# Kernel optimization log

Hardware: AMD Instinct MI355X
Metric: run time of the kernel (lower is better)

The kernel has to match this reference:

```python
import jax, jax.numpy as jnp
import numpy as np

D_MODEL = 64
D_STATE = 16
D_CONV = 4
EXPAND = 2
D_INNER = EXPAND * D_MODEL        # 128
DT_RANK = max(1, D_MODEL // 16)   # 4 (mamba_ssm default ceil(d_model/16))
BATCH, HH, WW = 2, 128, 128


def setup_inputs() -> dict:
    key = jax.random.key(0)
    ks = jax.random.split(key, 10)
    def norm(k, shape, sc=0.05):
        return jax.random.normal(k, shape, jnp.float32) * sc
    # A initialized as in mamba_ssm: A = 1..d_state per channel, stored as log
    A_log = jnp.log(jnp.tile(jnp.arange(1, D_STATE + 1, dtype=jnp.float32), (4, D_INNER, 1)))
    return {
        "x": jax.random.normal(ks[0], (BATCH, D_MODEL, HH, WW), jnp.float32),
        "in_w": norm(ks[1], (4, 2 * D_INNER, D_MODEL)),
        "conv_w": norm(ks[2], (4, D_INNER, D_CONV), 0.2),
        "conv_b": jnp.zeros((4, D_INNER), jnp.float32),
        "xp_w": norm(ks[3], (4, DT_RANK + 2 * D_STATE, D_INNER)),
        "dtp_w": norm(ks[4], (4, D_INNER, DT_RANK), 0.2),
        "dtp_b": jnp.full((4, D_INNER), -4.0, jnp.float32) + norm(ks[5], (4, D_INNER), 0.5),
        "A_log": A_log,
        "Dp": jnp.ones((4, D_INNER), jnp.float32),
        "out_w": norm(ks[6], (4, D_MODEL, D_INNER)),
        "fuse_w": norm(ks[7], (D_MODEL, 4 * D_MODEL)),
        "fuse_b": jnp.zeros((D_MODEL,), jnp.float32),
        "ln_g": jnp.ones((D_MODEL,), jnp.float32),
        "ln_b": jnp.zeros((D_MODEL,), jnp.float32),
    }


def _mamba(xseq, in_w, conv_w, conv_b, xp_w, dtp_w, dtp_b, A_log, Dp, out_w):
    # xseq: (N, L, d_model) -> (N, L, d_model). Single-direction Mamba block.
    N, L, _ = xseq.shape
    xz = xseq @ in_w.T                       # (N, L, 2*d_inner)
    u, z = jnp.split(xz, 2, axis=-1)
    # causal depthwise conv1d, kernel width D_CONV
    up = jnp.pad(u, ((0, 0), (D_CONV - 1, 0), (0, 0)))
    uc = conv_b + sum(up[:, k:k + L, :] * conv_w[:, k][None, None, :] for k in range(D_CONV))
    uc = jax.nn.silu(uc)
    dbl = uc @ xp_w.T                        # (N, L, dt_rank + 2*d_state)
    dt = jax.nn.softplus(dbl[..., :DT_RANK] @ dtp_w.T + dtp_b)   # (N, L, d_inner)
    Bm = dbl[..., DT_RANK:DT_RANK + D_STATE]                     # (N, L, d_state)
    Cm = dbl[..., DT_RANK + D_STATE:]                            # (N, L, d_state)
    A = -jnp.exp(A_log)                                          # (d_inner, d_state)

    def step(h, inp):
        dt_t, B_t, C_t, u_t = inp            # (N,d_inner),(N,d_state),(N,d_state),(N,d_inner)
        h = h * jnp.exp(dt_t[..., None] * A) + (dt_t * u_t)[..., None] * B_t[:, None, :]
        y = jnp.einsum('nds,ns->nd', h, C_t)
        return h, y

    h0 = jnp.zeros((N, D_INNER, D_STATE), xseq.dtype)
    _, ys = jax.lax.scan(step, h0, (dt.swapaxes(0, 1), Bm.swapaxes(0, 1),
                                    Cm.swapaxes(0, 1), uc.swapaxes(0, 1)))
    y = ys.swapaxes(0, 1) + uc * Dp
    y = y * jax.nn.silu(z)
    return y @ out_w.T


def reference(x, in_w, conv_w, conv_b, xp_w, dtp_w, dtp_b, A_log, Dp, out_w,
              fuse_w, fuse_b, ln_g, ln_b):
    B, C, H, W = x.shape
    xhwc = x.transpose(0, 2, 3, 1)           # (B,H,W,C)
    xwhc = x.transpose(0, 3, 2, 1)           # (B,W,H,C)
    d0 = xhwc.reshape(B * H, W, C)                         # horizontal fwd
    d1 = xhwc[:, :, ::-1, :].reshape(B * H, W, C)          # horizontal bwd
    d2 = xwhc.reshape(B * W, H, C)                         # vertical fwd
    d3 = xwhc[:, :, ::-1, :].reshape(B * W, H, C)          # vertical bwd
    xd = jnp.stack([d0, d1, d2, d3])         # (4, B*S, S, C) since H == W
    ys = jax.vmap(_mamba)(xd, in_w, conv_w, conv_b, xp_w, dtp_w, dtp_b, A_log, Dp, out_w)
    y0 = ys[0].reshape(B, H, W, C)
    y1 = ys[1].reshape(B, H, W, C)[:, :, ::-1, :]
    y2 = ys[2].reshape(B, W, H, C).transpose(0, 2, 1, 3)
    y3 = ys[3].reshape(B, W, H, C)[:, :, ::-1, :].transpose(0, 2, 1, 3)
    cat = jnp.concatenate([y0, y1, y2, y3], axis=-1)       # (B,H,W,4C)
    f = cat @ fuse_w.T + fuse_b                            # 1x1 conv
    mu = f.mean(-1, keepdims=True)
    var = f.var(-1, keepdims=True)
    f = (f - mu) * jax.lax.rsqrt(var + 1e-5) * ln_g + ln_b # LayerNorm over C
    f = jax.nn.silu(f)
    return f.transpose(0, 3, 1, 2)                          # (B,C,H,W)
```

## Files before the change

### kernel.cpp

```cpp
#include <hip/hip_runtime.h>
#include <hip/hip_bf16.h>
#include <math.h>


typedef __attribute__((ext_vector_type(8))) short short8;
typedef __attribute__((ext_vector_type(4))) float f32x4;
typedef __attribute__((ext_vector_type(2))) float f32x2;

__device__ __forceinline__ f32x2 pk_mul(f32x2 a, f32x2 b) {
  f32x2 d;
  asm("v_pk_mul_f32 %0, %1, %2" : "=v"(d) : "v"(a), "v"(b));
  return d;
}
__device__ __forceinline__ f32x2 pk_fma(f32x2 a, f32x2 b, f32x2 c) {
  f32x2 d;
  asm("v_pk_fma_f32 %0, %1, %2, %3" : "=v"(d) : "v"(a), "v"(b), "v"(c));
  return d;
}

__device__ __forceinline__ unsigned int pk2bf(float a, float b) {
  __hip_bfloat162 h = __float22bfloat162_rn(make_float2(a, b));
  unsigned int u;
  __builtin_memcpy(&u, &h, 4);
  return u;
}
__device__ __forceinline__ unsigned short f2bf(float f) {
  __hip_bfloat16 h = __float2bfloat16(f);
  unsigned short s;
  __builtin_memcpy(&s, &h, 2);
  return s;
}
__device__ __forceinline__ float bf2f(unsigned short h) {
  return __uint_as_float(((unsigned int)h) << 16);
}
__device__ __forceinline__ float fastrcp(float x) { return __builtin_amdgcn_rcpf(x); }
__device__ __forceinline__ float siluf(float x) { return x * fastrcp(1.f + __expf(-x)); }

__global__ void k0_prep(const float* __restrict__ out_w, const float* __restrict__ fuse_w,
                        const float* __restrict__ in_w, const float* __restrict__ xp_w,
                        const float* __restrict__ x,
                        unsigned short* __restrict__ MT16, unsigned short* __restrict__ W16,
                        unsigned short* __restrict__ XW16, unsigned short* __restrict__ XH,
                        unsigned short* __restrict__ XW) {
  __shared__ unsigned short sT[64*132];
  int blk = blockIdx.x;
  int tid = threadIdx.x;
  if (blk < 128) {
    int idx = blk * 256 + tid;
    int d   = idx & 127;
    int o   = (idx >> 7) & 63;
    int dir = idx >> 13;
    float acc = 0.f;
    #pragma unroll 8
    for (int j = 0; j < 64; ++j)
      acc += out_w[(dir*64 + j)*128 + d] * fuse_w[o*256 + dir*64 + j];
    MT16[o*512 + dir*128 + d] = f2bf(acc);
  } else if (blk < 160) {
    int t = (blk - 128) * 256 + tid;
    int base = t * 8;
    float4 v0 = *(const float4*)(in_w + base);
    float4 v1 = *(const float4*)(in_w + base + 4);
    uint4 pk;
    pk.x = pk2bf(v0.x, v0.y);
    pk.y = pk2bf(v0.z, v0.w);
    pk.z = pk2bf(v1.x, v1.y);
    pk.w = pk2bf(v1.z, v1.w);
    *(uint4*)(W16 + base) = pk;
  } else if (blk < 164) {
    int t = (blk - 160) * 256 + tid;
    for (int pid = t; pid < 4*48*128; pid += 1024) {
      int dir = pid / 6144;
      int rem = pid - dir*6144;
      int row = rem >> 7, c = rem & 127;
      XW16[pid] = (row < 36) ? f2bf(xp_w[dir*4608 + row*128 + c]) : (unsigned short)0;
    }
  } else {
    int idx = blk - 164;
    int b = idx >> 7, h = idx & 127;
    for (int f = tid*4; f < 8192; f += 1024) {
      int c = f >> 7, w = f & 127;
      float4 v = *(const float4*)(x + (((size_t)(b*64 + c)*128 + h)*128 + w));
      sT[c*132 + w + 0] = f2bf(v.x);
      sT[c*132 + w + 1] = f2bf(v.y);
      sT[c*132 + w + 2] = f2bf(v.z);
      sT[c*132 + w + 3] = f2bf(v.w);
    }
    __syncthreads();
    for (int f = tid*8; f < 8192; f += 2048) {
      int w = f >> 6, c0 = f & 63;
      unsigned int pk[4];
      #pragma unroll
      for (int p = 0; p < 4; ++p) {
        unsigned int lo = sT[(c0 + p*2 + 0)*132 + w];
        unsigned int hi = sT[(c0 + p*2 + 1)*132 + w];
        pk[p] = lo | (hi << 16);
      }
      uint4 v; v.x = pk[0]; v.y = pk[1]; v.z = pk[2]; v.w = pk[3];
      *(uint4*)(XH + (((size_t)(b*128 + h)*128 + w)*64 + c0)) = v;
      *(uint4*)(XW + (((size_t)(b*128 + w)*128 + h)*64 + c0)) = v;
    }
  }
}

__global__ __launch_bounds__(256, 3) void k1_front(
    const unsigned short* __restrict__ XH, const unsigned short* __restrict__ XW,
    const unsigned short* __restrict__ W16, const unsigned short* __restrict__ XW16,
    const float* __restrict__ conv_w, const float* __restrict__ conv_b,
    const float* __restrict__ dtp_w, const float* __restrict__ dtp_b,
    const float* __restrict__ A_log, const float* __restrict__ Dp,
    unsigned short* __restrict__ YF)
{
  __shared__ __align__(16) char smem[53248];
  float* sBCf         = (float*)smem;
  unsigned short* sUC = (unsigned short*)(smem + 18432);

  const int tid = threadIdx.x;
  const int dir = blockIdx.x >> 8;
  const int n   = blockIdx.x & 255;
  const int b   = n >> 7;
  const int r   = n & 127;
  const int n_all = dir*256 + n;

  const unsigned short* xsrc = (dir < 2 ? XH : XW) + ((size_t)(b*128 + r)*128)*64;

  const int wave = tid >> 6;
  const int lane = tid & 63;
  const int m16 = lane & 15;
  const int quad = lane >> 4;
  const int tb0 = wave * 32;
  const int st0 = tb0 + m16;
  const int st1 = tb0 + 16 + m16;
  const int sp0 = (dir & 1) ? (127 - st0) : st0;
  const int sp1 = (dir & 1) ? (127 - st1) : st1;

  unsigned int zpk[2][8][2];

  {
    short8 bfr[2][2];
    #pragma unroll
    for (int ks = 0; ks < 2; ++ks) {
      bfr[0][ks] = *(const short8*)(xsrc + sp0*64 + ks*32 + quad*8);
      bfr[1][ks] = *(const short8*)(xsrc + sp1*64 + ks*32 + quad*8);
    }
    const unsigned short* Wd = W16 + (size_t)dir * 16384;

    for (int rt = 0; rt < 8; ++rt) {
      short8 af[2];
      #pragma unroll
      for (int ks = 0; ks < 2; ++ks)
        af[ks] = *(const short8*)(Wd + (rt*16 + m16)*64 + ks*32 + quad*8);
      #pragma unroll
      for (int tt = 0; tt < 2; ++tt) {
        f32x4 acc = {0.f, 0.f, 0.f, 0.f};
        acc = __builtin_amdgcn_mfma_f32_16x16x32_bf16(af[0], bfr[tt][0], acc, 0, 0, 0);
        acc = __builtin_amdgcn_mfma_f32_16x16x32_bf16(af[1], bfr[tt][1], acc, 0, 0, 0);
        const int tok = tt ? st1 : st0;
        const int r0 = rt*16 + quad*4;
        uint2 u2;
        u2.x = pk2bf(acc[0], acc[1]);
        u2.y = pk2bf(acc[2], acc[3]);
        *(uint2*)(sUC + tok*136 + r0) = u2;
      }
    }
    #pragma unroll
    for (int k = 0; k < 8; ++k) {
      short8 af[2];
      #pragma unroll
      for (int ks = 0; ks < 2; ++ks)
        af[ks] = *(const short8*)(Wd + ((8+k)*16 + m16)*64 + ks*32 + quad*8);
      #pragma unroll
      for (int tt = 0; tt < 2; ++tt) {
        f32x4 acc = {0.f, 0.f, 0.f, 0.f};
        acc = __builtin_amdgcn_mfma_f32_16x16x32_bf16(af[0], bfr[tt][0], acc, 0, 0, 0);
        acc = __builtin_amdgcn_mfma_f32_16x16x32_bf16(af[1], bfr[tt][1], acc, 0, 0, 0);
        zpk[tt][k][0] = pk2bf(siluf(acc[0]), siluf(acc[1]));
        zpk[tt][k][1] = pk2bf(siluf(acc[2]), siluf(acc[3]));
      }
    }
  }
  __syncthreads();

  {
    const int d = tid & 127;
    const int half = tid >> 7;
    const int ca = half * 32;
    const int cb2 = (half + 2) * 32;
    const float* cw = conv_w + (size_t)(dir*128 + d)*4;
    const float c0w = cw[0], c1w = cw[1], c2w = cw[2], c3w = cw[3];
    const float cbv = conv_b[dir*128 + d];
    const f32x2 cw0v = {c0w, c0w}, cw1v = {c1w, c1w}, cw2v = {c2w, c2w}, cw3v = {c3w, c3w};
    const f32x2 cbv2 = {cbv, cbv};
    f32x2 A0 = { half ? bf2f(sUC[(ca-3)*136 + d]) : 0.f, bf2f(sUC[(cb2-3)*136 + d]) };
    f32x2 A1 = { half ? bf2f(sUC[(ca-2)*136 + d]) : 0.f, bf2f(sUC[(cb2-2)*136 + d]) };
    f32x2 A2 = { half ? bf2f(sUC[(ca-1)*136 + d]) : 0.f, bf2f(sUC[(cb2-1)*136 + d]) };
    __syncthreads();
    unsigned short* pa = sUC + ca*136 + d;
    unsigned short* pb = sUC + cb2*136 + d;
    for (int i = 0; i < 32; ++i) {
      f32x2 cur = { bf2f(*pa), bf2f(*pb) };
      f32x2 v = pk_fma(cw3v, cur,
                pk_fma(cw2v, A2,
                pk_fma(cw1v, A1,
                pk_fma(cw0v, A0, cbv2))));
      *pa = f2bf(siluf(v.x));
      *pb = f2bf(siluf(v.y));
      A0 = A1; A1 = A2; A2 = cur;
      pa += 136; pb += 136;
    }
  }
  __syncthreads();

  {
    short8 bfr[2][4];
    #pragma unroll
    for (int tt = 0; tt < 2; ++tt)
      #pragma unroll
      for (int ks = 0; ks < 4; ++ks)
        bfr[tt][ks] = *(const short8*)(sUC + (tt ? st1 : st0)*136 + ks*32 + quad*8);

    const unsigned short* XWd = XW16 + (size_t)dir * (48*128);

    for (int rt = 0; rt < 3; ++rt) {
      short8 af[4];
      #pragma unroll
      for (int ks = 0; ks < 4; ++ks)
        af[ks] = *(const short8*)(XWd + (rt*16 + m16)*128 + ks*32 + quad*8);
      #pragma unroll
      for (int tt = 0; tt < 2; ++tt) {
        f32x4 acc = {0.f, 0.f, 0.f, 0.f};
        #pragma unroll
        for (int ks = 0; ks < 4; ++ks)
          acc = __builtin_amdgcn_mfma_f32_16x16x32_bf16(af[ks], bfr[tt][ks], acc, 0, 0, 0);
        const int tok = tt ? st1 : st0;
        const int r0 = rt*16 + quad*4;
        if (r0 == 0) {
          float4 v; v.x = acc[0]; v.y = acc[1]; v.z = acc[2]; v.w = acc[3];
          *(float4*)(smem + 18432 + tok*272 + 256) = v;
        } else if (r0 < 36) {
          float4 v; v.x = acc[0]; v.y = acc[1]; v.z = acc[2]; v.w = acc[3];
          *(float4*)(sBCf + tok*36 + (r0 - 4)) = v;
        }
      }
    }
  }
  __syncthreads();

  {
    const int d = tid >> 1;
    const int p = tid & 1;
    const float* dwp = dtp_w + (size_t)(dir*128 + d) * 4;
    const float dw0 = dwp[0], dw1 = dwp[1], dw2 = dwp[2], dw3 = dwp[3];
    const float db = dtp_b[dir*128 + d];
    const float dpv = Dp[dir*128 + d];

    float Av[8];
    bool fast = true;
    #pragma unroll
    for (int j = 0; j < 8; ++j) {
      float a = -__expf(A_log[((size_t)(dir*128 + d))*16 + p*8 + j]);
      Av[j] = a;
      if (fabsf((-a) - (float)(p*8 + j + 1)) > 1e-3f) fast = false;
    }

    if (fast) {
      f32x2 h0 = {0.f, 0.f}, h1 = {0.f, 0.f}, h2v = {0.f, 0.f}, h3 = {0.f, 0.f};
      const char* qp = smem + 18432 + 256;
      const float* bp = sBCf + p*8;
      const float* cp = sBCf + 16 + p*8;
      const unsigned short* up = sUC + d;
      unsigned short* yo = sUC + d;
      for (int l = 0; l < 128; ++l) {
        float4 Q = *(const float4*)qp;
        f32x2 B01 = *(const f32x2*)(bp + 0), B23 = *(const f32x2*)(bp + 2);
        f32x2 B45 = *(const f32x2*)(bp + 4), B67 = *(const f32x2*)(bp + 6);
        f32x2 C01 = *(const f32x2*)(cp + 0), C23 = *(const f32x2*)(cp + 2);
        f32x2 C45 = *(const f32x2*)(cp + 4), C67 = *(const f32x2*)(cp + 6);
        float u = bf2f(*up);
        float dr = Q.x*dw0 + Q.y*dw1 + Q.z*dw2 + Q.w*dw3 + db;
        float te = __expf(dr);
        float dt = (dr > 20.f) ? dr : __logf(1.f + te);
        float dtu = dt * u;
        float E = fastrcp(1.f + te);
        float E2 = E*E, E4 = E2*E2, E8 = E4*E4;
        float eb = p ? E8 : 1.f;
        f32x2 P0 = {E*eb, E2*eb};
        f32x2 E2v = {E2, E2};
        f32x2 P1 = pk_mul(P0, E2v);
        f32x2 P2 = pk_mul(P1, E2v);
        f32x2 P3 = pk_mul(P2, E2v);
        f32x2 du = {dtu, dtu};
        h0  = pk_fma(h0,  P0, pk_mul(du, B01));
        h1  = pk_fma(h1,  P1, pk_mul(du, B23));
        h2v = pk_fma(h2v, P2, pk_mul(du, B45));
        h3  = pk_fma(h3,  P3, pk_mul(du, B67));
        f32x2 ya = pk_mul(h0, C01);
        f32x2 yb = pk_mul(h1, C23);
        ya = pk_fma(h2v, C45, ya);
        yb = pk_fma(h3,  C67, yb);
        float ypar = (ya.x + ya.y) + (yb.x + yb.y);
        float ot = __uint_as_float((unsigned int)__builtin_amdgcn_mov_dpp(
                     (int)__float_as_uint(ypar), 0xB1, 0xF, 0xF, true));
        float ysum = ypar + ot;
        *yo = f2bf(ysum + u*dpv);
        qp += 272; bp += 36; cp += 36; up += 136; yo += 136;
      }
    } else {
      float h[8];
      #pragma unroll
      for (int j = 0; j < 8; ++j) h[j] = 0.f;
      for (int l = 0; l < 128; ++l) {
        float4 Q = *(const float4*)(smem + 18432 + l*272 + 256);
        float4 b0 = *(const float4*)(sBCf + l*36 + p*8);
        float4 b1 = *(const float4*)(sBCf + l*36 + p*8 + 4);
        float4 c0 = *(const float4*)(sBCf + l*36 + 16 + p*8);
        float4 c1 = *(const float4*)(sBCf + l*36 + 16 + p*8 + 4);
        float Bv[8] = {b0.x,b0.y,b0.z,b0.w, b1.x,b1.y,b1.z,b1.w};
        float Cv[8] = {c0.x,c0.y,c0.z,c0.w, c1.x,c1.y,c1.z,c1.w};
        float u = bf2f(sUC[l*136 + d]);
        float dr = Q.x*dw0 + Q.y*dw1 + Q.z*dw2 + Q.w*dw3 + db;
        float te = __expf(dr);
        float dt = (dr > 20.f) ? dr : __logf(1.f + te);
        float dtu = dt * u;
        float yp = 0.f;
        #pragma unroll
        for (int j = 0; j < 8; ++j) {
          float ej = __expf(dt*Av[j]);
          h[j] = h[j]*ej + dtu*Bv[j];
          yp += h[j]*Cv[j];
        }
        float ot = __uint_as_float((unsigned int)__builtin_amdgcn_mov_dpp(
                     (int)__float_as_uint(yp), 0xB1, 0xF, 0xF, true));
        float ysum = yp + ot;
        if (p == 0) sUC[l*136 + d] = f2bf(ysum + u*dpv);
      }
    }
  }
  __syncthreads();

  #pragma unroll
  for (int tt = 0; tt < 2; ++tt) {
    const int st = tt ? st1 : st0;
    size_t rowbase;
    if (dir < 2)       rowbase = ((size_t)n_all*128 + st)*128;
    else if (dir == 2) rowbase = ((size_t)(512 + b*128 + st)*128 + r)*128;
    else               rowbase = ((size_t)(768 + b*128 + (127-st))*128 + r)*128;
    #pragma unroll
    for (int k = 0; k < 8; ++k) {
      const int dz = 16*k + quad*4;
      uint2 yv = *(const uint2*)(sUC + st*136 + dz);
      float y0 = __uint_as_float(yv.x << 16);
      float y1 = __uint_as_float(yv.x & 0xffff0000u);
      float y2 = __uint_as_float(yv.y << 16);
      float y3 = __uint_as_float(yv.y & 0xffff0000u);
      unsigned int z01 = zpk[tt][k][0], z23 = zpk[tt][k][1];
      float z0 = __uint_as_float(z01 << 16);
      float z1 = __uint_as_float(z01 & 0xffff0000u);
      float z2 = __uint_as_float(z23 << 16);
      float z3 = __uint_as_float(z23 & 0xffff0000u);
      uint2 ov;
      ov.x = pk2bf(y0*z0, y1*z1);
      ov.y = pk2bf(y2*z2, y3*z3);
      *(uint2*)(YF + rowbase + dz) = ov;
    }
  }
}

__global__ __launch_bounds__(512, 2) void k3_fuse(
    const unsigned short* __restrict__ YF, const unsigned short* __restrict__ MT16,
    const float* __restrict__ fuse_b, const float* __restrict__ ln_g,
    const float* __restrict__ ln_b, float* __restrict__ out)
{
  __shared__ __align__(16) unsigned short sYB[64*520];
  __shared__ float sLN[2][64][2];

  const int tid = threadIdx.x;
  const int blk = blockIdx.x;
  const int b = blk >> 8;
  const int rr2 = blk & 255;
  const int h = rr2 >> 1;
  const int w0 = (rr2 & 1) * 64;

  for (int f = tid*8; f < 32768; f += 4096) {
    int dirg = f >> 13;
    int rem = f & 8191;
    int tok = rem >> 7;
    int dd = rem & 127;
    int X = (dirg == 1) ? (127 - w0 - tok) : (w0 + tok);
    size_t base = ((size_t)(dirg*256 + b*128 + h)*128 + X)*128 + dd;
    *(uint4*)(sYB + tok*520 + dirg*128 + dd) = *(const uint4*)(YF + base);
  }
  __syncthreads();

  const int wave = tid >> 6;
  const int lane = tid & 63;
  const int m16 = lane & 15;
  const int quad = lane >> 4;
  const int tg   = wave & 3;
  const int mh   = wave >> 2;
  const int tok  = tg*16 + m16;

  short8 bfr[16];
  #pragma unroll
  for (int jt = 0; jt < 16; ++jt)
    bfr[jt] = *(const short8*)(sYB + tok*520 + jt*32 + quad*8);

  float facc[2][4];
  #pragma unroll
  for (int mi = 0; mi < 2; ++mi) {
    const int mt = mh*2 + mi;
    f32x4 acc = {0.f, 0.f, 0.f, 0.f};
    #pragma unroll
    for (int jt = 0; jt < 16; ++jt) {
      short8 af = *(const short8*)(MT16 + (size_t)(mt*16 + m16)*512 + jt*32 + quad*8);
      acc = __builtin_amdgcn_mfma_f32_16x16x32_bf16(af, bfr[jt], acc, 0, 0, 0);
    }
// ... 13 lines not shown
    }
  s1 += __shfl_xor(s1, 16, 64); s1 += __shfl_xor(s1, 32, 64);
  s2 += __shfl_xor(s2, 16, 64); s2 += __shfl_xor(s2, 32, 64);
  if (lane < 16) {
    sLN[mh][tok][0] = s1;
    sLN[mh][tok][1] = s2;
  }
  __syncthreads();
  float t1 = s1 + sLN[1 - mh][tok][0];
  float t2 = s2 + sLN[1 - mh][tok][1];
  float mu = t1 * (1.f/64.f);
  float var = t2 * (1.f/64.f) - mu*mu;
  float rs = rsqrtf(var + 1e-5f);

  #pragma unroll
  for (int mi = 0; mi < 2; ++mi)
    #pragma unroll
    for (int rr = 0; rr < 4; ++rr) {
      int o = (mh*2 + mi)*16 + quad*4 + rr;
      float v = (fv[mi*4 + rr] - mu) * rs * ln_g[o] + ln_b[o];
      out[((size_t)(b*64 + o)*128 + h)*128 + (w0 + tok)] = siluf(v);
    }
}

extern "C" void kernel_launch(void* const* d_in, const int* in_sizes, int n_in,
                              void* d_out, int out_size, void* d_ws, size_t ws_size,
                              hipStream_t stream) {
  const float* x      = (const float*)d_in[0];
  const float* in_w   = (const float*)d_in[1];
  const float* conv_w = (const float*)d_in[2];
  const float* conv_b = (const float*)d_in[3];
  const float* xp_w   = (const float*)d_in[4];
  const float* dtp_w  = (const float*)d_in[5];
  const float* dtp_b  = (const float*)d_in[6];
  const float* A_log  = (const float*)d_in[7];
  const float* Dp     = (const float*)d_in[8];
  const float* out_w  = (const float*)d_in[9];
  const float* fuse_w = (const float*)d_in[10];
  const float* fuse_b = (const float*)d_in[11];
  const float* ln_g   = (const float*)d_in[12];
  const float* ln_b   = (const float*)d_in[13];
  float* out = (float*)d_out;

  char* ws = (char*)d_ws;
  unsigned short* YF   = (unsigned short*)(ws);
  unsigned short* MT16 = (unsigned short*)(ws + 33554432);
  unsigned short* W16  = (unsigned short*)(ws + 33619968);
  unsigned short* XW16 = (unsigned short*)(ws + 33751040);
  unsigned short* XH   = (unsigned short*)(ws + 33800192);
  unsigned short* XWt  = (unsigned short*)(ws + 37994496);

  k0_prep<<<dim3(420), dim3(256), 0, stream>>>(out_w, fuse_w, in_w, xp_w, x,
                                               MT16, W16, XW16, XH, XWt);
  k1_front<<<dim3(1024), dim3(256), 0, stream>>>(XH, XWt, W16, XW16, conv_w, conv_b,
                                                 dtp_w, dtp_b, A_log, Dp, YF);
  k3_fuse<<<dim3(512), dim3(512), 0, stream>>>(YF, MT16, fuse_b, ln_g, ln_b, out);
}
```

Before: 203.5 us.

## Process two sequences per k1_front block, hoisting per-direction params and x_proj weights

k1_front now launches 512 blocks, and each block loops over two sequences of the same direction. The per-direction parameters (conv weights, dt_proj, A, D) and the x_proj weight fragments are loaded into registers once per block instead of once per sequence. Launch bounds drop from 3 to 2 blocks per SM to make room for the extra live registers. The cost is less occupancy and parallelism: 512 blocks on 256 CUs at 2 per CU fill only a single wave, so latency hiding may suffer.

```diff
diff --git a/kernel.cpp b/kernel.cpp
--- a/kernel.cpp
+++ b/kernel.cpp
@@ -102,7 +102,7 @@
   }
 }
 
-__global__ __launch_bounds__(256, 3) void k1_front(
+__global__ __launch_bounds__(256, 2) void k1_front(
     const unsigned short* __restrict__ XH, const unsigned short* __restrict__ XW,
     const unsigned short* __restrict__ W16, const unsigned short* __restrict__ XW16,
     const float* __restrict__ conv_w, const float* __restrict__ conv_b,
@@ -115,13 +115,8 @@
   unsigned short* sUC = (unsigned short*)(smem + 18432);
 
   const int tid = threadIdx.x;
-  const int dir = blockIdx.x >> 8;
-  const int n   = blockIdx.x & 255;
-  const int b   = n >> 7;
-  const int r   = n & 127;
-  const int n_all = dir*256 + n;
-
-  const unsigned short* xsrc = (dir < 2 ? XH : XW) + ((size_t)(b*128 + r)*128)*64;
+  const int dir = blockIdx.x >> 7;
+  const int n2  = blockIdx.x & 127;
 
   const int wave = tid >> 6;
   const int lane = tid & 63;
@@ -130,237 +125,251 @@
   const int tb0 = wave * 32;
   const int st0 = tb0 + m16;
   const int st1 = tb0 + 16 + m16;
-  const int sp0 = (dir & 1) ? (127 - st0) : st0;
-  const int sp1 = (dir & 1) ? (127 - st1) : st1;
-
-  unsigned int zpk[2][8][2];
-
-  {
-    short8 bfr[2][2];
+
+  const int cd = tid & 127;
+  const float* cwp = conv_w + (size_t)(dir*128 + cd)*4;
+  const float c0w = cwp[0], c1w = cwp[1], c2w = cwp[2], c3w = cwp[3];
+  const float cbv = conv_b[dir*128 + cd];
+  const int sd = tid >> 1;
+  const int sp_ = tid & 1;
+  const float* dwp = dtp_w + (size_t)(dir*128 + sd) * 4;
+  const float dw0 = dwp[0], dw1 = dwp[1], dw2 = dwp[2], dw3 = dwp[3];
+  const float db = dtp_b[dir*128 + sd];
+  const float dpv = Dp[dir*128 + sd];
+  float Av[8];
+  bool fast = true;
+  #pragma unroll
+  for (int j = 0; j < 8; ++j) {
+    float a = -__expf(A_log[((size_t)(dir*128 + sd))*16 + sp_*8 + j]);
+    Av[j] = a;
+    if (fabsf((-a) - (float)(sp_*8 + j + 1)) > 1e-3f) fast = false;
+  }
+  const unsigned short* XWd = XW16 + (size_t)dir * (48*128);
+  short8 af4[3][4];
+  #pragma unroll
+  for (int rt = 0; rt < 3; ++rt)
     #pragma unroll
-    for (int ks = 0; ks < 2; ++ks) {
-      bfr[0][ks] = *(const short8*)(xsrc + sp0*64 + ks*32 + quad*8);
-      bfr[1][ks] = *(const short8*)(xsrc + sp1*64 + ks*32 + quad*8);
-    }
-    const unsigned short* Wd = W16 + (size_t)dir * 16384;
-
-    for (int rt = 0; rt < 8; ++rt) {
-      short8 af[2];
-      #pragma unroll
-      for (int ks = 0; ks < 2; ++ks)
-        af[ks] = *(const short8*)(Wd + (rt*16 + m16)*64 + ks*32 + quad*8);
-      #pragma unroll
-      for (int tt = 0; tt < 2; ++tt) {
-        f32x4 acc = {0.f, 0.f, 0.f, 0.f};
-        acc = __builtin_amdgcn_mfma_f32_16x16x32_bf16(af[0], bfr[tt][0], acc, 0, 0, 0);
-        acc = __builtin_amdgcn_mfma_f32_16x16x32_bf16(af[1], bfr[tt][1], acc, 0, 0, 0);
-        const int tok = tt ? st1 : st0;
-        const int r0 = rt*16 + quad*4;
-        uint2 u2;
-        u2.x = pk2bf(acc[0], acc[1]);
-        u2.y = pk2bf(acc[2], acc[3]);
-        *(uint2*)(sUC + tok*136 + r0) = u2;
-      }
-    }
+    for (int ks = 0; ks < 4; ++ks)
+      af4[rt][ks] = *(const short8*)(XWd + (rt*16 + m16)*128 + ks*32 + quad*8);
+
+  const unsigned short* Wd = W16 + (size_t)dir * 16384;
+
+  for (int half = 0; half < 2; ++half) {
+    const int n = n2 + half*128;
+    const int b = n >> 7;
+    const int r = n & 127;
+    const int n_all = dir*256 + n;
+    const unsigned short* xsrc = (dir < 2 ? XH : XW) + ((size_t)(b*128 + r)*128)*64;
+    const int sp0 = (dir & 1) ? (127 - st0) : st0;
+    const int sp1 = (dir & 1) ? (127 - st1) : st1;
+
+    if (half) __syncthreads();
+
+    unsigned int zpk[2][8][2];
+
+    {
+      short8 bfr[2][2];
+      #pragma unroll
+      for (int ks = 0; ks < 2; ++ks) {
+        bfr[0][ks] = *(const short8*)(xsrc + sp0*64 + ks*32 + quad*8);
+        bfr[1][ks] = *(const short8*)(xsrc + sp1*64 + ks*32 + quad*8);
+      }
+      for (int rt = 0; rt < 8; ++rt) {
+        short8 af[2];
+        #pragma unroll
+        for (int ks = 0; ks < 2; ++ks)
+          af[ks] = *(const short8*)(Wd + (rt*16 + m16)*64 + ks*32 + quad*8);
+        #pragma unroll
+        for (int tt = 0; tt < 2; ++tt) {
+          f32x4 acc = {0.f, 0.f, 0.f, 0.f};
+          acc = __builtin_amdgcn_mfma_f32_16x16x32_bf16(af[0], bfr[tt][0], acc, 0, 0, 0);
+          acc = __builtin_amdgcn_mfma_f32_16x16x32_bf16(af[1], bfr[tt][1], acc, 0, 0, 0);
+          const int tok = tt ? st1 : st0;
+          const int r0 = rt*16 + quad*4;
+          uint2 u2;
+          u2.x = pk2bf(acc[0], acc[1]);
+          u2.y = pk2bf(acc[2], acc[3]);
+          *(uint2*)(sUC + tok*136 + r0) = u2;
+        }
+      }
+      #pragma unroll
+      for (int k = 0; k < 8; ++k) {
+        short8 af[2];
+        #pragma unroll
+        for (int ks = 0; ks < 2; ++ks)
+          af[ks] = *(const short8*)(Wd + ((8+k)*16 + m16)*64 + ks*32 + quad*8);
+        #pragma unroll
+        for (int tt = 0; tt < 2; ++tt) {
+          f32x4 acc = {0.f, 0.f, 0.f, 0.f};
+          acc = __builtin_amdgcn_mfma_f32_16x16x32_bf16(af[0], bfr[tt][0], acc, 0, 0, 0);
+          acc = __builtin_amdgcn_mfma_f32_16x16x32_bf16(af[1], bfr[tt][1], acc, 0, 0, 0);
+          zpk[tt][k][0] = pk2bf(siluf(acc[0]), siluf(acc[1]));
+          zpk[tt][k][1] = pk2bf(siluf(acc[2]), siluf(acc[3]));
+        }
+      }
+    }
+    __syncthreads();
+
+    {
+      const int d = cd;
+      const int hlf = tid >> 7;
+      const int ca = hlf * 32;
+      const int cb2 = (hlf + 2) * 32;
+      const f32x2 cw0v = {c0w, c0w}, cw1v = {c1w, c1w}, cw2v = {c2w, c2w}, cw3v = {c3w, c3w};
+      const f32x2 cbv2 = {cbv, cbv};
+      f32x2 A0 = { hlf ? bf2f(sUC[(ca-3)*136 + d]) : 0.f, bf2f(sUC[(cb2-3)*136 + d]) };
+      f32x2 A1 = { hlf ? bf2f(sUC[(ca-2)*136 + d]) : 0.f, bf2f(sUC[(cb2-2)*136 + d]) };
+      f32x2 A2 = { hlf ? bf2f(sUC[(ca-1)*136 + d]) : 0.f, bf2f(sUC[(cb2-1)*136 + d]) };
+      __syncthreads();
+      unsigned short* pa = sUC + ca*136 + d;
+      unsigned short* pb = sUC + cb2*136 + d;
+      for (int i = 0; i < 32; ++i) {
+        f32x2 cur = { bf2f(*pa), bf2f(*pb) };
+        f32x2 v = pk_fma(cw3v, cur,
+                  pk_fma(cw2v, A2,
+                  pk_fma(cw1v, A1,
+                  pk_fma(cw0v, A0, cbv2))));
+        *pa = f2bf(siluf(v.x));
+        *pb = f2bf(siluf(v.y));
+        A0 = A1; A1 = A2; A2 = cur;
+        pa += 136; pb += 136;
+      }
+    }
+    __syncthreads();
+
+    {
+      short8 bfr[2][4];
+      #pragma unroll
+      for (int tt = 0; tt < 2; ++tt)
+        #pragma unroll
+        for (int ks = 0; ks < 4; ++ks)
+          bfr[tt][ks] = *(const short8*)(sUC + (tt ? st1 : st0)*136 + ks*32 + quad*8);
+
+      #pragma unroll
+      for (int rt = 0; rt < 3; ++rt) {
+        #pragma unroll
+        for (int tt = 0; tt < 2; ++tt) {
+          f32x4 acc = {0.f, 0.f, 0.f, 0.f};
+          #pragma unroll
+          for (int ks = 0; ks < 4; ++ks)
+            acc = __builtin_amdgcn_mfma_f32_16x16x32_bf16(af4[rt][ks], bfr[tt][ks], acc, 0, 0, 0);
+          const int tok = tt ? st1 : st0;
+          const int r0 = rt*16 + quad*4;
+          if (r0 == 0) {
+            float4 v; v.x = acc[0]; v.y = acc[1]; v.z = acc[2]; v.w = acc[3];
+            *(float4*)(smem + 18432 + tok*272 + 256) = v;
+          } else if (r0 < 36) {
+            float4 v; v.x = acc[0]; v.y = acc[1]; v.z = acc[2]; v.w = acc[3];
+            *(float4*)(sBCf + tok*36 + (r0 - 4)) = v;
+          }
+        }
+      }
+    }
+    __syncthreads();
+
+    {
+      const int d = sd;
+      const int p = sp_;
+      if (fast) {
+        f32x2 h0 = {0.f, 0.f}, h1 = {0.f, 0.f}, h2v = {0.f, 0.f}, h3 = {0.f, 0.f};
+        const char* qp = smem + 18432 + 256;
+        const float* bp = sBCf + p*8;
+        const float* cp = sBCf + 16 + p*8;
+        const unsigned short* up = sUC + d;
+        unsigned short* yo = sUC + d;
+        for (int l = 0; l < 128; ++l) {
+          float4 Q = *(const float4*)qp;
+          f32x2 B01 = *(const f32x2*)(bp + 0), B23 = *(const f32x2*)(bp + 2);
+          f32x2 B45 = *(const f32x2*)(bp + 4), B67 = *(const f32x2*)(bp + 6);
+          f32x2 C01 = *(const f32x2*)(cp + 0), C23 = *(const f32x2*)(cp + 2);
+          f32x2 C45 = *(const f32x2*)(cp + 4), C67 = *(const f32x2*)(cp + 6);
+          float u = bf2f(*up);
+          float dr = Q.x*dw0 + Q.y*dw1 + Q.z*dw2 + Q.w*dw3 + db;
+          float te = __expf(dr);
+          float dt = (dr > 20.f) ? dr : __logf(1.f + te);
+          float dtu = dt * u;
+          float E = fastrcp(1.f + te);
+          float E2 = E*E, E4 = E2*E2, E8 = E4*E4;
+          float eb = p ? E8 : 1.f;
+          f32x2 P0 = {E*eb, E2*eb};
+          f32x2 E2v = {E2, E2};
+          f32x2 P1 = pk_mul(P0, E2v);
+          f32x2 P2 = pk_mul(P1, E2v);
+          f32x2 P3 = pk_mul(P2, E2v);
+          f32x2 du = {dtu, dtu};
+          h0  = pk_fma(h0,  P0, pk_mul(du, B01));
+          h1  = pk_fma(h1,  P1, pk_mul(du, B23));
+          h2v = pk_fma(h2v, P2, pk_mul(du, B45));
+          h3  = pk_fma(h3,  P3, pk_mul(du, B67));
+          f32x2 ya = pk_mul(h0, C01);
+          f32x2 yb = pk_mul(h1, C23);
+          ya = pk_fma(h2v, C45, ya);
+          yb = pk_fma(h3,  C67, yb);
+          float ypar = (ya.x + ya.y) + (yb.x + yb.y);
+          float ot = __uint_as_float((unsigned int)__builtin_amdgcn_mov_dpp(
+                       (int)__float_as_uint(ypar), 0xB1, 0xF, 0xF, true));
+          float ysum = ypar + ot;
+          *yo = f2bf(ysum + u*dpv);
+          qp += 272; bp += 36; cp += 36; up += 136; yo += 136;
+        }
+      } else {
+        float h[8];
+        #pragma unroll
+        for (int j = 0; j < 8; ++j) h[j] = 0.f;
+        for (int l = 0; l < 128; ++l) {
+          float4 Q = *(const float4*)(smem + 18432 + l*272 + 256);
+          float4 b0 = *(const float4*)(sBCf + l*36 + p*8);
+          float4 b1 = *(const float4*)(sBCf + l*36 + p*8 + 4);
+          float4 c0 = *(const float4*)(sBCf + l*36 + 16 + p*8);
+          float4 c1 = *(const float4*)(sBCf + l*36 + 16 + p*8 + 4);
+          float Bv[8] = {b0.x,b0.y,b0.z,b0.w, b1.x,b1.y,b1.z,b1.w};
+          float Cv[8] = {c0.x,c0.y,c0.z,c0.w, c1.x,c1.y,c1.z,c1.w};
+          float u = bf2f(sUC[l*136 + d]);
+          float dr = Q.x*dw0 + Q.y*dw1 + Q.z*dw2 + Q.w*dw3 + db;
+          float te = __expf(dr);
+          float dt = (dr > 20.f) ? dr : __logf(1.f + te);
+          float dtu = dt * u;
+          float yp = 0.f;
+          #pragma unroll
+          for (int j = 0; j < 8; ++j) {
+            float ej = __expf(dt*Av[j]);
+            h[j] = h[j]*ej + dtu*Bv[j];
+            yp += h[j]*Cv[j];
+          }
+          float ot = __uint_as_float((unsigned int)__builtin_amdgcn_mov_dpp(
+                       (int)__float_as_uint(yp), 0xB1, 0xF, 0xF, true));
+          float ysum = yp + ot;
+          if (p == 0) sUC[l*136 + d] = f2bf(ysum + u*dpv);
+        }
+      }
+    }
+    __syncthreads();
+
     #pragma unroll
-    for (int k = 0; k < 8; ++k) {
-      short8 af[2];
-      #pragma unroll
-      for (int ks = 0; ks < 2; ++ks)
-        af[ks] = *(const short8*)(Wd + ((8+k)*16 + m16)*64 + ks*32 + quad*8);
-      #pragma unroll
-      for (int tt = 0; tt < 2; ++tt) {
-        f32x4 acc = {0.f, 0.f, 0.f, 0.f};
-        acc = __builtin_amdgcn_mfma_f32_16x16x32_bf16(af[0], bfr[tt][0], acc, 0, 0, 0);
-        acc = __builtin_amdgcn_mfma_f32_16x16x32_bf16(af[1], bfr[tt][1], acc, 0, 0, 0);
-        zpk[tt][k][0] = pk2bf(siluf(acc[0]), siluf(acc[1]));
-        zpk[tt][k][1] = pk2bf(siluf(acc[2]), siluf(acc[3]));
-      }
-    }
-  }
-  __syncthreads();
-
-  {
-    const int d = tid & 127;
-    const int half = tid >> 7;
-    const int ca = half * 32;
-    const int cb2 = (half + 2) * 32;
-    const float* cw = conv_w + (size_t)(dir*128 + d)*4;
-    const float c0w = cw[0], c1w = cw[1], c2w = cw[2], c3w = cw[3];
-    const float cbv = conv_b[dir*128 + d];
-    const f32x2 cw0v = {c0w, c0w}, cw1v = {c1w, c1w}, cw2v = {c2w, c2w}, cw3v = {c3w, c3w};
-    const f32x2 cbv2 = {cbv, cbv};
-    f32x2 A0 = { half ? bf2f(sUC[(ca-3)*136 + d]) : 0.f, bf2f(sUC[(cb2-3)*136 + d]) };
-    f32x2 A1 = { half ? bf2f(sUC[(ca-2)*136 + d]) : 0.f, bf2f(sUC[(cb2-2)*136 + d]) };
-    f32x2 A2 = { half ? bf2f(sUC[(ca-1)*136 + d]) : 0.f, bf2f(sUC[(cb2-1)*136 + d]) };
-    __syncthreads();
-    unsigned short* pa = sUC + ca*136 + d;
-    unsigned short* pb = sUC + cb2*136 + d;
-    for (int i = 0; i < 32; ++i) {
-      f32x2 cur = { bf2f(*pa), bf2f(*pb) };
-      f32x2 v = pk_fma(cw3v, cur,
-                pk_fma(cw2v, A2,
-                pk_fma(cw1v, A1,
-                pk_fma(cw0v, A0, cbv2))));
-      *pa = f2bf(siluf(v.x));
-      *pb = f2bf(siluf(v.y));
-      A0 = A1; A1 = A2; A2 = cur;
-      pa += 136; pb += 136;
-    }
-  }
-  __syncthreads();
-
-  {
-    short8 bfr[2][4];
-    #pragma unroll
-    for (int tt = 0; tt < 2; ++tt)
-      #pragma unroll
-      for (int ks = 0; ks < 4; ++ks)
-        bfr[tt][ks] = *(const short8*)(sUC + (tt ? st1 : st0)*136 + ks*32 + quad*8);
-
-    const unsigned short* XWd = XW16 + (size_t)dir * (48*128);
-
-    for (int rt = 0; rt < 3; ++rt) {
-      short8 af[4];
-      #pragma unroll
-      for (int ks = 0; ks < 4; ++ks)
-        af[ks] = *(const short8*)(XWd + (rt*16 + m16)*128 + ks*32 + quad*8);
-      #pragma unroll
-      for (int tt = 0; tt < 2; ++tt) {
-        f32x4 acc = {0.f, 0.f, 0.f, 0.f};
-        #pragma unroll
-        for (int ks = 0; ks < 4; ++ks)
-          acc = __builtin_amdgcn_mfma_f32_16x16x32_bf16(af[ks], bfr[tt][ks], acc, 0, 0, 0);
-        const int tok = tt ? st1 : st0;
-        const int r0 = rt*16 + quad*4;
-        if (r0 == 0) {
-          float4 v; v.x = acc[0]; v.y = acc[1]; v.z = acc[2]; v.w = acc[3];
-          *(float4*)(smem + 18432 + tok*272 + 256) = v;
-        } else if (r0 < 36) {
-          float4 v; v.x = acc[0]; v.y = acc[1]; v.z = acc[2]; v.w = acc[3];
-          *(float4*)(sBCf + tok*36 + (r0 - 4)) = v;
-        }
-      }
-    }
-  }
-  __syncthreads();
-
-  {
-    const int d = tid >> 1;
-    const int p = tid & 1;
-    const float* dwp = dtp_w + (size_t)(dir*128 + d) * 4;
-    const float dw0 = dwp[0], dw1 = dwp[1], dw2 = dwp[2], dw3 = dwp[3];
-    const float db = dtp_b[dir*128 + d];
-    const float dpv = Dp[dir*128 + d];
-
-    float Av[8];
-    bool fast = true;
-    #pragma unroll
-    for (int j = 0; j < 8; ++j) {
-      float a = -__expf(A_log[((size_t)(dir*128 + d))*16 + p*8 + j]);
-      Av[j] = a;
-      if (fabsf((-a) - (float)(p*8 + j + 1)) > 1e-3f) fast = false;
-    }
-
-    if (fast) {
-      f32x2 h0 = {0.f, 0.f}, h1 = {0.f, 0.f}, h2v = {0.f, 0.f}, h3 = {0.f, 0.f};
-      const char* qp = smem + 18432 + 256;
-      const float* bp = sBCf + p*8;
-      const float* cp = sBCf + 16 + p*8;
-      const unsigned short* up = sUC + d;
-      unsigned short* yo = sUC + d;
-      for (int l = 0; l < 128; ++l) {
-        float4 Q = *(const float4*)qp;
-        f32x2 B01 = *(const f32x2*)(bp + 0), B23 = *(const f32x2*)(bp + 2);
-        f32x2 B45 = *(const f32x2*)(bp + 4), B67 = *(const f32x2*)(bp + 6);
-        f32x2 C01 = *(const f32x2*)(cp + 0), C23 = *(const f32x2*)(cp + 2);
-        f32x2 C45 = *(const f32x2*)(cp + 4), C67 = *(const f32x2*)(cp + 6);
-        float u = bf2f(*up);
-        float dr = Q.x*dw0 + Q.y*dw1 + Q.z*dw2 + Q.w*dw3 + db;
-        float te = __expf(dr);
-        float dt = (dr > 20.f) ? dr : __logf(1.f + te);
-        float dtu = dt * u;
-        float E = fastrcp(1.f + te);
-        float E2 = E*E, E4 = E2*E2, E8 = E4*E4;
-        float eb = p ? E8 : 1.f;
-        f32x2 P0 = {E*eb, E2*eb};
-        f32x2 E2v = {E2, E2};
-        f32x2 P1 = pk_mul(P0, E2v);
-        f32x2 P2 = pk_mul(P1, E2v);
-        f32x2 P3 = pk_mul(P2, E2v);
-        f32x2 du = {dtu, dtu};
-        h0  = pk_fma(h0,  P0, pk_mul(du, B01));
-        h1  = pk_fma(h1,  P1, pk_mul(du, B23));
-        h2v = pk_fma(h2v, P2, pk_mul(du, B45));
-        h3  = pk_fma(h3,  P3, pk_mul(du, B67));
-        f32x2 ya = pk_mul(h0, C01);
-        f32x2 yb = pk_mul(h1, C23);
-        ya = pk_fma(h2v, C45, ya);
-        yb = pk_fma(h3,  C67, yb);
-        float ypar = (ya.x + ya.y) + (yb.x + yb.y);
-        float ot = __uint_as_float((unsigned int)__builtin_amdgcn_mov_dpp(
-                     (int)__float_as_uint(ypar), 0xB1, 0xF, 0xF, true));
-        float ysum = ypar + ot;
-        *yo = f2bf(ysum + u*dpv);
-        qp += 272; bp += 36; cp += 36; up += 136; yo += 136;
-      }
-    } else {
-      float h[8];
-      #pragma unroll
-      for (int j = 0; j < 8; ++j) h[j] = 0.f;
-      for (int l = 0; l < 128; ++l) {
-        float4 Q = *(const float4*)(smem + 18432 + l*272 + 256);
-        float4 b0 = *(const float4*)(sBCf + l*36 + p*8);
-        float4 b1 = *(const float4*)(sBCf + l*36 + p*8 + 4);
-        float4 c0 = *(const float4*)(sBCf + l*36 + 16 + p*8);
-        float4 c1 = *(const float4*)(sBCf + l*36 + 16 + p*8 + 4);
-        float Bv[8] = {b0.x,b0.y,b0.z,b0.w, b1.x,b1.y,b1.z,b1.w};
-        float Cv[8] = {c0.x,c0.y,c0.z,c0.w, c1.x,c1.y,c1.z,c1.w};
-        float u = bf2f(sUC[l*136 + d]);
-        float dr = Q.x*dw0 + Q.y*dw1 + Q.z*dw2 + Q.w*dw3 + db;
-        float te = __expf(dr);
-        float dt = (dr > 20.f) ? dr : __logf(1.f + te);
-        float dtu = dt * u;
-        float yp = 0.f;
-        #pragma unroll
-        for (int j = 0; j < 8; ++j) {
-          float ej = __expf(dt*Av[j]);
-          h[j] = h[j]*ej + dtu*Bv[j];
-          yp += h[j]*Cv[j];
-        }
-        float ot = __uint_as_float((unsigned int)__builtin_amdgcn_mov_dpp(
-                     (int)__float_as_uint(yp), 0xB1, 0xF, 0xF, true));
-        float ysum = yp + ot;
-        if (p == 0) sUC[l*136 + d] = f2bf(ysum + u*dpv);
-      }
-    }
-  }
-  __syncthreads();
-
-  #pragma unroll
-  for (int tt = 0; tt < 2; ++tt) {
-    const int st = tt ? st1 : st0;
-    size_t rowbase;
-    if (dir < 2)       rowbase = ((size_t)n_all*128 + st)*128;
-    else if (dir == 2) rowbase = ((size_t)(512 + b*128 + st)*128 + r)*128;
-    else               rowbase = ((size_t)(768 + b*128 + (127-st))*128 + r)*128;
-    #pragma unroll
-    for (int k = 0; k < 8; ++k) {
-      const int dz = 16*k + quad*4;
-      uint2 yv = *(const uint2*)(sUC + st*136 + dz);
-      float y0 = __uint_as_float(yv.x << 16);
-      float y1 = __uint_as_float(yv.x & 0xffff0000u);
-      float y2 = __uint_as_float(yv.y << 16);
-      float y3 = __uint_as_float(yv.y & 0xffff0000u);
-      unsigned int z01 = zpk[tt][k][0], z23 = zpk[tt][k][1];
-      float z0 = __uint_as_float(z01 << 16);
-      float z1 = __uint_as_float(z01 & 0xffff0000u);
-      float z2 = __uint_as_float(z23 << 16);
-      float z3 = __uint_as_float(z23 & 0xffff0000u);
-      uint2 ov;
-      ov.x = pk2bf(y0*z0, y1*z1);
-      ov.y = pk2bf(y2*z2, y3*z3);
-      *(uint2*)(YF + rowbase + dz) = ov;
+    for (int tt = 0; tt < 2; ++tt) {
+      const int st = tt ? st1 : st0;
+      size_t rowbase;
+      if (dir < 2)       rowbase = ((size_t)n_all*128 + st)*128;
+      else if (dir == 2) rowbase = ((size_t)(512 + b*128 + st)*128 + r)*128;
+      else               rowbase = ((size_t)(768 + b*128 + (127-st))*128 + r)*128;
+      #pragma unroll
+      for (int k = 0; k < 8; ++k) {
+        const int dz = 16*k + quad*4;
+        uint2 yv = *(const uint2*)(sUC + st*136 + dz);
+        float y0 = __uint_as_float(yv.x << 16);
+        float y1 = __uint_as_float(yv.x & 0xffff0000u);
+        float y2 = __uint_as_float(yv.y << 16);
+        float y3 = __uint_as_float(yv.y & 0xffff0000u);
+        unsigned int z01 = zpk[tt][k][0], z23 = zpk[tt][k][1];
+        float z0 = __uint_as_float(z01 << 16);
+        float z1 = __uint_as_float(z01 & 0xffff0000u);
+        float z2 = __uint_as_float(z23 << 16);
+        float z3 = __uint_as_float(z23 & 0xffff0000u);
+        uint2 ov;
+        ov.x = pk2bf(y0*z0, y1*z1);
+        ov.y = pk2bf(y2*z2, y3*z3);
+        *(uint2*)(YF + rowbase + dz) = ov;
+      }
     }
   }
 }
@@ -480,7 +489,7 @@
 
   k0_prep<<<dim3(420), dim3(256), 0, stream>>>(out_w, fuse_w, in_w, xp_w, x,
                                                MT16, W16, XW16, XH, XWt);
-  k1_front<<<dim3(1024), dim3(256), 0, stream>>>(XH, XWt, W16, XW16, conv_w, conv_b,
-                                                 dtp_w, dtp_b, A_log, Dp, YF);
+  k1_front<<<dim3(512), dim3(256), 0, stream>>>(XH, XWt, W16, XW16, conv_w, conv_b,
+                                                dtp_w, dtp_b, A_log, Dp, YF);
   k3_fuse<<<dim3(512), dim3(512), 0, stream>>>(YF, MT16, fuse_b, ln_g, ln_b, out);
 }
```

Result: slower. 246.8 us (+21.3%).

## Split selective scan into two sequence chunks with state carry-over correction

Applied to the files above, without the earlier changes.

Doubles k1_front block size to 512 threads so each wave handles 16 tokens instead of 32. The selective scan is split into two 64-token chunks run in parallel. The second chunk starts from zero state, and a correction pass then adds the first chunk's propagated final state using cumulative decay products. This relies on A being 1..16 so that exp(dt*A) equals powers of a single factor. The aim is to halve the serial scan length and raise occupancy, at the cost of an extra sync, a correction loop, and more LDS.

```diff
diff --git a/kernel.cpp b/kernel.cpp
--- a/kernel.cpp
+++ b/kernel.cpp
@@ -35,6 +35,10 @@
 }
 __device__ __forceinline__ float fastrcp(float x) { return __builtin_amdgcn_rcpf(x); }
 __device__ __forceinline__ float siluf(float x) { return x * fastrcp(1.f + __expf(-x)); }
+__device__ __forceinline__ float dpp_swap1(float x) {
+  return __uint_as_float((unsigned int)__builtin_amdgcn_mov_dpp(
+           (int)__float_as_uint(x), 0xB1, 0xF, 0xF, true));
+}
 
 __global__ void k0_prep(const float* __restrict__ out_w, const float* __restrict__ fuse_w,
                         const float* __restrict__ in_w, const float* __restrict__ xp_w,
@@ -102,7 +106,7 @@
   }
 }
 
-__global__ __launch_bounds__(256, 3) void k1_front(
+__global__ __launch_bounds__(512, 4) void k1_front(
     const unsigned short* __restrict__ XH, const unsigned short* __restrict__ XW,
     const unsigned short* __restrict__ W16, const unsigned short* __restrict__ XW16,
     const float* __restrict__ conv_w, const float* __restrict__ conv_b,
@@ -110,9 +114,10 @@
     const float* __restrict__ A_log, const float* __restrict__ Dp,
     unsigned short* __restrict__ YF)
 {
-  __shared__ __align__(16) char smem[53248];
+  __shared__ __align__(16) char smem[61440];
   float* sBCf         = (float*)smem;
   unsigned short* sUC = (unsigned short*)(smem + 18432);
+  float* hbuf         = (float*)(smem + 53248);
 
   const int tid = threadIdx.x;
   const int dir = blockIdx.x >> 8;
@@ -127,21 +132,16 @@
   const int lane = tid & 63;
   const int m16 = lane & 15;
   const int quad = lane >> 4;
-  const int tb0 = wave * 32;
-  const int st0 = tb0 + m16;
-  const int st1 = tb0 + 16 + m16;
-  const int sp0 = (dir & 1) ? (127 - st0) : st0;
-  const int sp1 = (dir & 1) ? (127 - st1) : st1;
-
-  unsigned int zpk[2][8][2];
+  const int st = wave*16 + m16;
+  const int sp = (dir & 1) ? (127 - st) : st;
+
+  unsigned int zpk[8][2];
 
   {
-    short8 bfr[2][2];
-    #pragma unroll
-    for (int ks = 0; ks < 2; ++ks) {
-      bfr[0][ks] = *(const short8*)(xsrc + sp0*64 + ks*32 + quad*8);
-      bfr[1][ks] = *(const short8*)(xsrc + sp1*64 + ks*32 + quad*8);
-    }
+    short8 bfr[2];
+    #pragma unroll
+    for (int ks = 0; ks < 2; ++ks)
+      bfr[ks] = *(const short8*)(xsrc + sp*64 + ks*32 + quad*8);
     const unsigned short* Wd = W16 + (size_t)dir * 16384;
 
     for (int rt = 0; rt < 8; ++rt) {
@@ -149,18 +149,14 @@
       #pragma unroll
       for (int ks = 0; ks < 2; ++ks)
         af[ks] = *(const short8*)(Wd + (rt*16 + m16)*64 + ks*32 + quad*8);
-      #pragma unroll
-      for (int tt = 0; tt < 2; ++tt) {
-        f32x4 acc = {0.f, 0.f, 0.f, 0.f};
-        acc = __builtin_amdgcn_mfma_f32_16x16x32_bf16(af[0], bfr[tt][0], acc, 0, 0, 0);
-        acc = __builtin_amdgcn_mfma_f32_16x16x32_bf16(af[1], bfr[tt][1], acc, 0, 0, 0);
-        const int tok = tt ? st1 : st0;
-        const int r0 = rt*16 + quad*4;
-        uint2 u2;
-        u2.x = pk2bf(acc[0], acc[1]);
-        u2.y = pk2bf(acc[2], acc[3]);
-        *(uint2*)(sUC + tok*136 + r0) = u2;
-      }
+      f32x4 acc = {0.f, 0.f, 0.f, 0.f};
+      acc = __builtin_amdgcn_mfma_f32_16x16x32_bf16(af[0], bfr[0], acc, 0, 0, 0);
+      acc = __builtin_amdgcn_mfma_f32_16x16x32_bf16(af[1], bfr[1], acc, 0, 0, 0);
+      const int r0 = rt*16 + quad*4;
+      uint2 u2;
+      u2.x = pk2bf(acc[0], acc[1]);
+      u2.y = pk2bf(acc[2], acc[3]);
+      *(uint2*)(sUC + st*136 + r0) = u2;
     }
     #pragma unroll
     for (int k = 0; k < 8; ++k) {
@@ -168,55 +164,42 @@
       #pragma unroll
       for (int ks = 0; ks < 2; ++ks)
         af[ks] = *(const short8*)(Wd + ((8+k)*16 + m16)*64 + ks*32 + quad*8);
-      #pragma unroll
-      for (int tt = 0; tt < 2; ++tt) {
-        f32x4 acc = {0.f, 0.f, 0.f, 0.f};
-        acc = __builtin_amdgcn_mfma_f32_16x16x32_bf16(af[0], bfr[tt][0], acc, 0, 0, 0);
-        acc = __builtin_amdgcn_mfma_f32_16x16x32_bf16(af[1], bfr[tt][1], acc, 0, 0, 0);
-        zpk[tt][k][0] = pk2bf(siluf(acc[0]), siluf(acc[1]));
-        zpk[tt][k][1] = pk2bf(siluf(acc[2]), siluf(acc[3]));
-      }
+      f32x4 acc = {0.f, 0.f, 0.f, 0.f};
+      acc = __builtin_amdgcn_mfma_f32_16x16x32_bf16(af[0], bfr[0], acc, 0, 0, 0);
+      acc = __builtin_amdgcn_mfma_f32_16x16x32_bf16(af[1], bfr[1], acc, 0, 0, 0);
+      zpk[k][0] = pk2bf(siluf(acc[0]), siluf(acc[1]));
+      zpk[k][1] = pk2bf(siluf(acc[2]), siluf(acc[3]));
     }
   }
   __syncthreads();
 
   {
     const int d = tid & 127;
-    const int half = tid >> 7;
-    const int ca = half * 32;
-    const int cb2 = (half + 2) * 32;
+    const int c4 = tid >> 7;
+    const int ca = c4 * 32;
     const float* cw = conv_w + (size_t)(dir*128 + d)*4;
     const float c0w = cw[0], c1w = cw[1], c2w = cw[2], c3w = cw[3];
     const float cbv = conv_b[dir*128 + d];
-    const f32x2 cw0v = {c0w, c0w}, cw1v = {c1w, c1w}, cw2v = {c2w, c2w}, cw3v = {c3w, c3w};
-    const f32x2 cbv2 = {cbv, cbv};
-    f32x2 A0 = { half ? bf2f(sUC[(ca-3)*136 + d]) : 0.f, bf2f(sUC[(cb2-3)*136 + d]) };
-    f32x2 A1 = { half ? bf2f(sUC[(ca-2)*136 + d]) : 0.f, bf2f(sUC[(cb2-2)*136 + d]) };
-    f32x2 A2 = { half ? bf2f(sUC[(ca-1)*136 + d]) : 0.f, bf2f(sUC[(cb2-1)*136 + d]) };
+    float a0 = c4 ? bf2f(sUC[(ca-3)*136 + d]) : 0.f;
+    float a1 = c4 ? bf2f(sUC[(ca-2)*136 + d]) : 0.f;
+    float a2 = c4 ? bf2f(sUC[(ca-1)*136 + d]) : 0.f;
     __syncthreads();
     unsigned short* pa = sUC + ca*136 + d;
-    unsigned short* pb = sUC + cb2*136 + d;
     for (int i = 0; i < 32; ++i) {
-      f32x2 cur = { bf2f(*pa), bf2f(*pb) };
-      f32x2 v = pk_fma(cw3v, cur,
-                pk_fma(cw2v, A2,
-                pk_fma(cw1v, A1,
-                pk_fma(cw0v, A0, cbv2))));
-      *pa = f2bf(siluf(v.x));
-      *pb = f2bf(siluf(v.y));
-      A0 = A1; A1 = A2; A2 = cur;
-      pa += 136; pb += 136;
+      float cur = bf2f(*pa);
+      float v = cbv + c0w*a0 + c1w*a1 + c2w*a2 + c3w*cur;
+      *pa = f2bf(siluf(v));
+      a0 = a1; a1 = a2; a2 = cur;
+      pa += 136;
     }
   }
   __syncthreads();
 
   {
-    short8 bfr[2][4];
-    #pragma unroll
-    for (int tt = 0; tt < 2; ++tt)
-      #pragma unroll
-      for (int ks = 0; ks < 4; ++ks)
-        bfr[tt][ks] = *(const short8*)(sUC + (tt ? st1 : st0)*136 + ks*32 + quad*8);
+    short8 bfr[4];
+    #pragma unroll
+    for (int ks = 0; ks < 4; ++ks)
+      bfr[ks] = *(const short8*)(sUC + st*136 + ks*32 + quad*8);
 
     const unsigned short* XWd = XW16 + (size_t)dir * (48*128);
 
@@ -225,29 +208,26 @@
       #pragma unroll
       for (int ks = 0; ks < 4; ++ks)
         af[ks] = *(const short8*)(XWd + (rt*16 + m16)*128 + ks*32 + quad*8);
+      f32x4 acc = {0.f, 0.f, 0.f, 0.f};
       #pragma unroll
-      for (int tt = 0; tt < 2; ++tt) {
-        f32x4 acc = {0.f, 0.f, 0.f, 0.f};
-        #pragma unroll
-        for (int ks = 0; ks < 4; ++ks)
-          acc = __builtin_amdgcn_mfma_f32_16x16x32_bf16(af[ks], bfr[tt][ks], acc, 0, 0, 0);
-        const int tok = tt ? st1 : st0;
-        const int r0 = rt*16 + quad*4;
-        if (r0 == 0) {
-          float4 v; v.x = acc[0]; v.y = acc[1]; v.z = acc[2]; v.w = acc[3];
-          *(float4*)(smem + 18432 + tok*272 + 256) = v;
-        } else if (r0 < 36) {
-          float4 v; v.x = acc[0]; v.y = acc[1]; v.z = acc[2]; v.w = acc[3];
-          *(float4*)(sBCf + tok*36 + (r0 - 4)) = v;
-        }
+      for (int ks = 0; ks < 4; ++ks)
+        acc = __builtin_amdgcn_mfma_f32_16x16x32_bf16(af[ks], bfr[ks], acc, 0, 0, 0);
+      const int r0 = rt*16 + quad*4;
+      if (r0 == 0) {
+        float4 v; v.x = acc[0]; v.y = acc[1]; v.z = acc[2]; v.w = acc[3];
+        *(float4*)(smem + 18432 + st*272 + 256) = v;
+      } else if (r0 < 36) {
+        float4 v; v.x = acc[0]; v.y = acc[1]; v.z = acc[2]; v.w = acc[3];
+        *(float4*)(sBCf + st*36 + (r0 - 4)) = v;
       }
     }
   }
   __syncthreads();
 
   {
-    const int d = tid >> 1;
     const int p = tid & 1;
+    const int d = (tid >> 1) & 127;
+    const int c = tid >> 8;
     const float* dwp = dtp_w + (size_t)(dir*128 + d) * 4;
     const float dw0 = dwp[0], dw1 = dwp[1], dw2 = dwp[2], dw3 = dwp[3];
     const float db = dtp_b[dir*128 + d];
@@ -264,12 +244,12 @@
 
     if (fast) {
       f32x2 h0 = {0.f, 0.f}, h1 = {0.f, 0.f}, h2v = {0.f, 0.f}, h3 = {0.f, 0.f};
-      const char* qp = smem + 18432 + 256;
-      const float* bp = sBCf + p*8;
-      const float* cp = sBCf + 16 + p*8;
-      const unsigned short* up = sUC + d;
-      unsigned short* yo = sUC + d;
-      for (int l = 0; l < 128; ++l) {
+      const char* qp = smem + 18432 + 256 + c*64*272;
+      const float* bp = sBCf + c*64*36 + p*8;
+      const float* cp = sBCf + c*64*36 + 16 + p*8;
+      const unsigned short* up = sUC + c*64*136 + d;
+      unsigned short* yo = sUC + c*64*136 + d;
+      for (int l = 0; l < 64; ++l) {
         float4 Q = *(const float4*)qp;
         f32x2 B01 = *(const f32x2*)(bp + 0), B23 = *(const f32x2*)(bp + 2);
         f32x2 B45 = *(const f32x2*)(bp + 4), B67 = *(const f32x2*)(bp + 6);
@@ -298,13 +278,19 @@
         ya = pk_fma(h2v, C45, ya);
         yb = pk_fma(h3,  C67, yb);
         float ypar = (ya.x + ya.y) + (yb.x + yb.y);
-        float ot = __uint_as_float((unsigned int)__builtin_amdgcn_mov_dpp(
-                     (int)__float_as_uint(ypar), 0xB1, 0xF, 0xF, true));
+        float ot = dpp_swap1(ypar);
         float ysum = ypar + ot;
         *yo = f2bf(ysum + u*dpv);
         qp += 272; bp += 36; cp += 36; up += 136; yo += 136;
       }
-    } else {
+      if (c == 0) {
+        float* hb = hbuf + d*16 + p*8;
+        *(f32x2*)(hb + 0) = h0;
+        *(f32x2*)(hb + 2) = h1;
+        *(f32x2*)(hb + 4) = h2v;
+        *(f32x2*)(hb + 6) = h3;
+      }
+    } else if (c == 0) {
       float h[8];
       #pragma unroll
       for (int j = 0; j < 8; ++j) h[j] = 0.f;
@@ -328,18 +314,53 @@
           h[j] = h[j]*ej + dtu*Bv[j];
           yp += h[j]*Cv[j];
         }
-        float ot = __uint_as_float((unsigned int)__builtin_amdgcn_mov_dpp(
-                     (int)__float_as_uint(yp), 0xB1, 0xF, 0xF, true));
+        float ot = dpp_swap1(yp);
         float ysum = yp + ot;
         if (p == 0) sUC[l*136 + d] = f2bf(ysum + u*dpv);
       }
     }
+    __syncthreads();
+
+    if (fast && c == 1) {
+      const float* hb = hbuf + d*16 + p*8;
+      f32x2 hin01 = *(const f32x2*)(hb + 0);
+      f32x2 hin23 = *(const f32x2*)(hb + 2);
+      f32x2 hin45 = *(const f32x2*)(hb + 4);
+      f32x2 hin67 = *(const f32x2*)(hb + 6);
+      float G = 1.f;
+      const char* qp = smem + 18432 + 256 + 64*272;
+      const float* cp = sBCf + 64*36 + 16 + p*8;
+      unsigned short* yo = sUC + 64*136 + d;
+      for (int l = 0; l < 64; ++l) {
+        float4 Q = *(const float4*)qp;
+        float dr = Q.x*dw0 + Q.y*dw1 + Q.z*dw2 + Q.w*dw3 + db;
+        float te = __expf(dr);
+        float E = fastrcp(1.f + te);
+        G *= E;
+        float G2 = G*G, G4 = G2*G2, G8 = G4*G4;
+        float eb = p ? G8 : 1.f;
+        f32x2 P0 = {G*eb, G2*eb};
+        f32x2 G2v = {G2, G2};
+        f32x2 P1 = pk_mul(P0, G2v);
+        f32x2 P2 = pk_mul(P1, G2v);
+        f32x2 P3 = pk_mul(P2, G2v);
+        f32x2 C01 = *(const f32x2*)(cp + 0), C23 = *(const f32x2*)(cp + 2);
+        f32x2 C45 = *(const f32x2*)(cp + 4), C67 = *(const f32x2*)(cp + 6);
+        f32x2 a = pk_mul(pk_mul(P0, hin01), C01);
+        a = pk_fma(pk_mul(P1, hin23), C23, a);
+        a = pk_fma(pk_mul(P2, hin45), C45, a);
+        a = pk_fma(pk_mul(P3, hin67), C67, a);
+        float corr = a.x + a.y;
+        float ot = dpp_swap1(corr);
+        corr += ot;
+        *yo = f2bf(bf2f(*yo) + corr);
+        qp += 272; cp += 36; yo += 136;
+      }
+    }
   }
   __syncthreads();
 
-  #pragma unroll
-  for (int tt = 0; tt < 2; ++tt) {
-    const int st = tt ? st1 : st0;
+  {
     size_t rowbase;
     if (dir < 2)       rowbase = ((size_t)n_all*128 + st)*128;
     else if (dir == 2) rowbase = ((size_t)(512 + b*128 + st)*128 + r)*128;
@@ -352,7 +373,7 @@
       float y1 = __uint_as_float(yv.x & 0xffff0000u);
       float y2 = __uint_as_float(yv.y << 16);
       float y3 = __uint_as_float(yv.y & 0xffff0000u);
-      unsigned int z01 = zpk[tt][k][0], z23 = zpk[tt][k][1];
+      unsigned int z01 = zpk[k][0], z23 = zpk[k][1];
       float z0 = __uint_as_float(z01 << 16);
       float z1 = __uint_as_float(z01 & 0xffff0000u);
       float z2 = __uint_as_float(z23 << 16);
@@ -480,7 +501,7 @@
 
   k0_prep<<<dim3(420), dim3(256), 0, stream>>>(out_w, fuse_w, in_w, xp_w, x,
                                                MT16, W16, XW16, XH, XWt);
-  k1_front<<<dim3(1024), dim3(256), 0, stream>>>(XH, XWt, W16, XW16, conv_w, conv_b,
+  k1_front<<<dim3(1024), dim3(512), 0, stream>>>(XH, XWt, W16, XW16, conv_w, conv_b,
                                                  dtp_w, dtp_b, A_log, Dp, YF);
   k3_fuse<<<dim3(512), dim3(512), 0, stream>>>(YF, MT16, fuse_b, ln_g, ln_b, out);
 }
```

After: 232.9 us. 14.5% more time.
